# Kernel tuning notes

Measured on AMD Instinct MI355X. Metric: run time of the kernel, lower is better.

Reference implementation:

```python
import jax, jax.numpy as jnp
import numpy as np
from jax import lax

DILATION = 2


def setup_inputs() -> dict:
    key = jax.random.key(0)
    k1, k2, k3 = jax.random.split(key, 3)
    x = jax.random.normal(k1, (2048, 4096), dtype=jnp.float32)      # [T, num_inputs]
    weights = jax.random.normal(k2, (32, 16), dtype=jnp.float32)    # [num_lags, num_filters]
    biases = jax.random.normal(k3, (16,), dtype=jnp.float32) * 0.1  # [num_filters]
    return {"x": x, "weights": weights, "biases": biases}


def reference(x, weights, biases):
    T, num_inputs = x.shape
    L, F = weights.shape  # num_lags, num_filters

    # pos_constraint: clip weights at 0; normalize_weights: l2-normalize over lag axis
    w_p = jnp.maximum(weights, 0.0)
    w_pn = w_p * lax.rsqrt(jnp.maximum(jnp.sum(w_p * w_p, axis=0, keepdims=True), 1e-12))

    # reverse in time, pad num_lags zeros at the end -> causal filter of length 2L
    padded_filt = jnp.concatenate([w_pn[::-1], jnp.zeros((L, F), dtype=w_pn.dtype)], axis=0)
    kernel = padded_filt.reshape(2 * L, 1, 1, F)  # HWIO

    # [T, num_inputs] -> transpose -> [num_inputs, T, 1, 1] (NHWC, batch = input units)
    shaped_input = x.T.reshape(num_inputs, T, 1, 1)

    pre = lax.conv_general_dilated(
        shaped_input, kernel,
        window_strides=(1, 1),
        padding='SAME',
        rhs_dilation=(DILATION, 1),
        dimension_numbers=('NHWC', 'HWIO', 'NHWC'),
    )  # [num_inputs, T, 1, F]

    post = jax.nn.relu(pre + biases)  # bias broadcast over filters, relu activation

    # transpose to [T, num_inputs, 1, F] -> [T, num_inputs*F]
    out = jnp.transpose(post, (1, 0, 2, 3)).reshape(T, num_inputs * F)
    return out
```

## Files before the change

### kernel.cpp

```cpp
#include <hip/hip_runtime.h>


constexpr int T = 2048;
constexpr int N = 4096;
constexpr int L = 32;
constexpr int F = 16;
constexpr int BT = 64;
constexpr int BN = 64;
constexpr int ROWS = BT + 62;
constexpr int OUT_STRIDE = N * F;

typedef float vf4 __attribute__((ext_vector_type(4)));

__global__ __launch_bounds__(256, 2)
void tlayer_kernel(const float* __restrict__ x,
                   const float* __restrict__ w,
                   const float* __restrict__ bias,
                   float* __restrict__ out)
{
    __shared__ float sx[ROWS * BN];
    __shared__ float sw[L * F];
    __shared__ float sscale[F];

    const int tid = threadIdx.x;
    const int n0  = blockIdx.x * BN;
    const int t0  = blockIdx.y * BT;

    sw[tid]       = fmaxf(w[tid], 0.f);
    sw[tid + 256] = fmaxf(w[tid + 256], 0.f);
    __syncthreads();
    if (tid < F) {
        float s = 0.f;
        #pragma unroll
        for (int l = 0; l < L; ++l) { float v = sw[l * F + tid]; s += v * v; }
        sscale[tid] = rsqrtf(fmaxf(s, 1e-12f));
    }
    __syncthreads();
    sw[tid]       *= sscale[tid & 15];
    sw[tid + 256] *= sscale[tid & 15];

    for (int idx = tid; idx < ROWS * (BN / 4); idx += 256) {
        const int r  = idx >> 4;
        const int c4 = idx & 15;
        const int g  = t0 - 63 + r;
        float4 v = make_float4(0.f, 0.f, 0.f, 0.f);
        if (g >= 0 && g < T)
            v = *(const float4*)(x + (size_t)g * N + n0 + c4 * 4);
        *(float4*)(sx + r * BN + c4 * 4) = v;
    }
    __syncthreads();

    const int f4 = tid & 3;
    const int nl = tid >> 2;
    const float4 b4 = *(const float4*)(bias + f4 * 4);

    float4 wr[L];
    #pragma unroll
    for (int l = 0; l < L; ++l)
        wr[l] = *(const float4*)(sw + l * F + f4 * 4);

    float* outbase = out + (size_t)(n0 + nl) * F + f4 * 4;

    for (int grp = 0; grp < 16; ++grp) {
        const int toff = (grp & 1) + (grp >> 1) * 8;

        float xv[35];
        const int base = toff * BN + nl;
        #pragma unroll
        for (int m = 0; m < 35; ++m)
            xv[m] = sx[base + m * (2 * BN)];

        float4 acc[4] = {b4, b4, b4, b4};
        #pragma unroll
        for (int l = 0; l < L; ++l) {
            const float4 w4 = wr[l];
            #pragma unroll
            for (int j = 0; j < 4; ++j) {
                const float xs = xv[31 + j - l];
                acc[j].x = fmaf(xs, w4.x, acc[j].x);
                acc[j].y = fmaf(xs, w4.y, acc[j].y);
                acc[j].z = fmaf(xs, w4.z, acc[j].z);
                acc[j].w = fmaf(xs, w4.w, acc[j].w);
            }
        }

        #pragma unroll
        for (int j = 0; j < 4; ++j) {
            vf4 r;
            r.x = fmaxf(acc[j].x, 0.f);
            r.y = fmaxf(acc[j].y, 0.f);
            r.z = fmaxf(acc[j].z, 0.f);
            r.w = fmaxf(acc[j].w, 0.f);
            __builtin_nontemporal_store(
                r, (vf4*)(outbase + (size_t)(t0 + toff + 2 * j) * OUT_STRIDE));
        }
    }
}

extern "C" void kernel_launch(void* const* d_in, const int* in_sizes, int n_in,
                              void* d_out, int out_size, void* d_ws, size_t ws_size,
                              hipStream_t stream) {
    const float* x    = (const float*)d_in[0];
    const float* w    = (const float*)d_in[1];
    const float* bias = (const float*)d_in[2];
    float* out = (float*)d_out;

    dim3 grid(N / BN, T / BT);
    tlayer_kernel<<<grid, 256, 0, stream>>>(x, w, bias, out);
}
```

Measured before the change: 553.4 us.

## Transpose x tile into parity-split shared layout, vectorize loads, halve tile width

Stores the x tile in shared memory transposed and split by time parity, with padded rows, so each thread reads its dilated time window with contiguous 16-byte LDS loads instead of 35 scalar strided reads. Each thread now handles 2 filters instead of 4, with 32 input columns per block, and the launch bound asks for 4 blocks per CU to raise occupancy. The cost is a scatter-style transposed store into shared memory, narrower 8-byte output stores, and twice as many blocks each reloading the weights and the overlapping x halo.

```diff
diff --git a/kernel.cpp b/kernel.cpp
--- a/kernel.cpp
+++ b/kernel.cpp
@@ -6,19 +6,20 @@
 constexpr int L = 32;
 constexpr int F = 16;
 constexpr int BT = 64;
-constexpr int BN = 64;
-constexpr int ROWS = BT + 62;
+constexpr int BN = 32;
+constexpr int RP = 68;
 constexpr int OUT_STRIDE = N * F;
 
-typedef float vf4 __attribute__((ext_vector_type(4)));
+typedef float f4 __attribute__((ext_vector_type(4)));
+typedef float f2 __attribute__((ext_vector_type(2)));
 
-__global__ __launch_bounds__(256, 2)
+__global__ __launch_bounds__(256, 4)
 void tlayer_kernel(const float* __restrict__ x,
                    const float* __restrict__ w,
                    const float* __restrict__ bias,
                    float* __restrict__ out)
 {
-    __shared__ float sx[ROWS * BN];
+    __shared__ __align__(16) float sxT[2 * BN * RP];
     __shared__ float sw[L * F];
     __shared__ float sscale[F];
 
@@ -39,60 +40,81 @@
     sw[tid]       *= sscale[tid & 15];
     sw[tid + 256] *= sscale[tid & 15];
 
-    for (int idx = tid; idx < ROWS * (BN / 4); idx += 256) {
-        const int r  = idx >> 4;
-        const int c4 = idx & 15;
+    for (int idx = tid; idx < 126 * (BN / 4); idx += 256) {
+        const int r  = idx >> 3;
+        const int c4 = idx & 7;
         const int g  = t0 - 63 + r;
-        float4 v = make_float4(0.f, 0.f, 0.f, 0.f);
+        f4 v = {0.f, 0.f, 0.f, 0.f};
         if (g >= 0 && g < T)
-            v = *(const float4*)(x + (size_t)g * N + n0 + c4 * 4);
-        *(float4*)(sx + r * BN + c4 * 4) = v;
+            v = *(const f4*)(x + (size_t)g * N + n0 + c4 * 4);
+        const int p  = r & 1;
+        const int rr = r >> 1;
+        float* dst = sxT + p * (BN * RP) + (c4 * 4) * RP + rr;
+        dst[0 * RP] = v[0];
+        dst[1 * RP] = v[1];
+        dst[2 * RP] = v[2];
+        dst[3 * RP] = v[3];
     }
     __syncthreads();
 
-    const int f4 = tid & 3;
-    const int nl = tid >> 2;
-    const float4 b4 = *(const float4*)(bias + f4 * 4);
+    const int fp = tid & 7;
+    const int nl = tid >> 3;
+    const f2 b2 = *(const f2*)(bias + fp * 2);
 
-    float4 wr[L];
+    f2 wr[L];
     #pragma unroll
     for (int l = 0; l < L; ++l)
-        wr[l] = *(const float4*)(sw + l * F + f4 * 4);
+        wr[l] = *(const f2*)(sw + l * F + fp * 2);
 
-    float* outbase = out + (size_t)(n0 + nl) * F + f4 * 4;
+    const float* myrow = sxT + nl * RP;
+    float* outbase = out + (size_t)(n0 + nl) * F + fp * 2;
 
+    #pragma unroll 1
     for (int grp = 0; grp < 16; ++grp) {
         const int toff = (grp & 1) + (grp >> 1) * 8;
+        const int p    = grp & 1;
+        const int r0p  = (grp >> 1) * 4;
+        const float* src = myrow + p * (BN * RP) + r0p;
 
-        float xv[35];
-        const int base = toff * BN + nl;
+        f2 acc[4] = {b2, b2, b2, b2};
+
+        f4 xa[5];
         #pragma unroll
-        for (int m = 0; m < 35; ++m)
-            xv[m] = sx[base + m * (2 * BN)];
+        for (int u = 0; u < 5; ++u)
+            xa[u] = *(const f4*)(src + 4 * u);
 
-        float4 acc[4] = {b4, b4, b4, b4};
         #pragma unroll
-        for (int l = 0; l < L; ++l) {
-            const float4 w4 = wr[l];
+        for (int l = 16; l < 32; ++l) {
+            const f2 wl = wr[l];
             #pragma unroll
             for (int j = 0; j < 4; ++j) {
-                const float xs = xv[31 + j - l];
-                acc[j].x = fmaf(xs, w4.x, acc[j].x);
-                acc[j].y = fmaf(xs, w4.y, acc[j].y);
-                acc[j].z = fmaf(xs, w4.z, acc[j].z);
-                acc[j].w = fmaf(xs, w4.w, acc[j].w);
+                const int m = 31 + j - l;
+                acc[j] += wl * xa[m >> 2][m & 3];
+            }
+        }
+
+        f4 xb[5];
+        #pragma unroll
+        for (int u = 0; u < 5; ++u)
+            xb[u] = *(const f4*)(src + 16 + 4 * u);
+
+        #pragma unroll
+        for (int l = 0; l < 16; ++l) {
+            const f2 wl = wr[l];
+            #pragma unroll
+            for (int j = 0; j < 4; ++j) {
+                const int k = 15 + j - l;
+                acc[j] += wl * xb[k >> 2][k & 3];
             }
         }
 
         #pragma unroll
         for (int j = 0; j < 4; ++j) {
-            vf4 r;
-            r.x = fmaxf(acc[j].x, 0.f);
-            r.y = fmaxf(acc[j].y, 0.f);
-            r.z = fmaxf(acc[j].z, 0.f);
-            r.w = fmaxf(acc[j].w, 0.f);
+            f2 r;
+            r[0] = fmaxf(acc[j][0], 0.f);
+            r[1] = fmaxf(acc[j][1], 0.f);
             __builtin_nontemporal_store(
-                r, (vf4*)(outbase + (size_t)(t0 + toff + 2 * j) * OUT_STRIDE));
+                r, (f2*)(outbase + (size_t)(t0 + toff + 2 * j) * OUT_STRIDE));
         }
     }
 }
```

After: 548.8 us. Within noise of the previous version (-0.8%).

## Restructure into parity-split time tiles with register-resident accumulators over 16 outputs

Applied to the files above, without the earlier changes.

Each block now handles one time parity and 16 dilated output steps (32-row span) for 64 inputs, loading only the 47 same-parity input rows into padded shared memory, which halves the x staging per block. Each thread streams the rows once and accumulates 16 outputs in registers, replacing the per-group 35-value reload loop. The grid is flattened to one dimension, the row stride is padded to cut bank conflicts, and nontemporal stores become plain stores. The cost is smaller tiles with a larger halo relative to work, more blocks, and higher register pressure from 16 float4 accumulators plus 32 weight vectors.

```diff
diff --git a/kernel.cpp b/kernel.cpp
--- a/kernel.cpp
+++ b/kernel.cpp
@@ -5,12 +5,13 @@
 constexpr int N = 4096;
 constexpr int L = 32;
 constexpr int F = 16;
-constexpr int BT = 64;
 constexpr int BN = 64;
-constexpr int ROWS = BT + 62;
+constexpr int KT = 16;
+constexpr int NR = 47;
+constexpr int RP = 68;
 constexpr int OUT_STRIDE = N * F;
 
-typedef float vf4 __attribute__((ext_vector_type(4)));
+typedef float f4 __attribute__((ext_vector_type(4)));
 
 __global__ __launch_bounds__(256, 2)
 void tlayer_kernel(const float* __restrict__ x,
@@ -18,13 +19,16 @@
                    const float* __restrict__ bias,
                    float* __restrict__ out)
 {
-    __shared__ float sx[ROWS * BN];
+    __shared__ __align__(16) float sxs[NR * RP];
     __shared__ float sw[L * F];
     __shared__ float sscale[F];
 
-    const int tid = threadIdx.x;
-    const int n0  = blockIdx.x * BN;
-    const int t0  = blockIdx.y * BT;
+    const int tid  = threadIdx.x;
+    const int bi   = blockIdx.x;
+    const int ngrp = bi & 63;
+    const int tg   = bi >> 6;
+    const int t0   = (tg & 1) + (tg >> 1) * 32;
+    const int n0   = ngrp * BN;
 
     sw[tid]       = fmaxf(w[tid], 0.f);
     sw[tid + 256] = fmaxf(w[tid + 256], 0.f);
@@ -39,61 +43,51 @@
     sw[tid]       *= sscale[tid & 15];
     sw[tid + 256] *= sscale[tid & 15];
 
-    for (int idx = tid; idx < ROWS * (BN / 4); idx += 256) {
+    for (int idx = tid; idx < NR * 16; idx += 256) {
         const int r  = idx >> 4;
         const int c4 = idx & 15;
-        const int g  = t0 - 63 + r;
-        float4 v = make_float4(0.f, 0.f, 0.f, 0.f);
-        if (g >= 0 && g < T)
-            v = *(const float4*)(x + (size_t)g * N + n0 + c4 * 4);
-        *(float4*)(sx + r * BN + c4 * 4) = v;
+        const int g  = t0 - 63 + 2 * r;
+        f4 v = {0.f, 0.f, 0.f, 0.f};
+        if (g >= 0)
+            v = *(const f4*)(x + (size_t)g * N + n0 + c4 * 4);
+        *(f4*)(&sxs[r * RP + c4 * 4]) = v;
     }
     __syncthreads();
 
-    const int f4 = tid & 3;
+    const int fq = tid & 3;
     const int nl = tid >> 2;
-    const float4 b4 = *(const float4*)(bias + f4 * 4);
 
-    float4 wr[L];
+    f4 wr[L];
     #pragma unroll
     for (int l = 0; l < L; ++l)
-        wr[l] = *(const float4*)(sw + l * F + f4 * 4);
+        wr[l] = *(const f4*)(sw + l * F + fq * 4);
 
-    float* outbase = out + (size_t)(n0 + nl) * F + f4 * 4;
+    const f4 b4 = *(const f4*)(bias + fq * 4);
+    f4 acc[KT];
+    #pragma unroll
+    for (int i = 0; i < KT; ++i) acc[i] = b4;
 
-    for (int grp = 0; grp < 16; ++grp) {
-        const int toff = (grp & 1) + (grp >> 1) * 8;
-
-        float xv[35];
-        const int base = toff * BN + nl;
+    const float* xp = sxs + nl;
+    #pragma unroll
+    for (int r = 0; r < NR; ++r) {
+        const float xv = xp[r * RP];
         #pragma unroll
-        for (int m = 0; m < 35; ++m)
-            xv[m] = sx[base + m * (2 * BN)];
-
-        float4 acc[4] = {b4, b4, b4, b4};
-        #pragma unroll
-        for (int l = 0; l < L; ++l) {
-            const float4 w4 = wr[l];
-            #pragma unroll
-            for (int j = 0; j < 4; ++j) {
-                const float xs = xv[31 + j - l];
-                acc[j].x = fmaf(xs, w4.x, acc[j].x);
-                acc[j].y = fmaf(xs, w4.y, acc[j].y);
-                acc[j].z = fmaf(xs, w4.z, acc[j].z);
-                acc[j].w = fmaf(xs, w4.w, acc[j].w);
+        for (int i = 0; i < KT; ++i) {
+            if (r >= i && r <= 31 + i) {
+                acc[i] += wr[31 + i - r] * xv;
             }
         }
+    }
 
-        #pragma unroll
-        for (int j = 0; j < 4; ++j) {
-            vf4 r;
-            r.x = fmaxf(acc[j].x, 0.f);
-            r.y = fmaxf(acc[j].y, 0.f);
-            r.z = fmaxf(acc[j].z, 0.f);
-            r.w = fmaxf(acc[j].w, 0.f);
-            __builtin_nontemporal_store(
-                r, (vf4*)(outbase + (size_t)(t0 + toff + 2 * j) * OUT_STRIDE));
-        }
+    float* ob = out + (size_t)(n0 + nl) * F + fq * 4;
+    #pragma unroll
+    for (int i = 0; i < KT; ++i) {
+        f4 v;
+        v[0] = fmaxf(acc[i][0], 0.f);
+        v[1] = fmaxf(acc[i][1], 0.f);
+        v[2] = fmaxf(acc[i][2], 0.f);
+        v[3] = fmaxf(acc[i][3], 0.f);
+        *(f4*)(ob + (size_t)(t0 + 2 * i) * OUT_STRIDE) = v;
     }
 }
 
@@ -105,6 +99,6 @@
     const float* bias = (const float*)d_in[2];
     float* out = (float*)d_out;
 
-    dim3 grid(N / BN, T / BT);
+    dim3 grid(128 * 64);
     tlayer_kernel<<<grid, 256, 0, stream>>>(x, w, bias, out);
 }
```

Measured after the change: 561.7 us. About the same (+1.5%).
